# Performance work log

Hardware: AMD Instinct MI355X
Metric: run time of the kernel (lower is better)

## Reference

```python
import jax, jax.numpy as jnp
import numpy as np

B, L, DIM = 2, 1024, 512
HEADS = 8
D = DIM // HEADS
FORE_DIM, POST_DIM = 256, 1024
L_FORE, L_POST = 4 * L, L // 4


def setup_inputs() -> dict:
    key = jax.random.key(0)
    ks = jax.random.split(key, 8)
    s = 0.02  # weight init scale
    return {
        "x": jax.random.normal(ks[0], (B, L, DIM), jnp.float32),
        "fore_x": jax.random.normal(ks[1], (B, L_FORE, FORE_DIM), jnp.float32),
        "post_x": jax.random.normal(ks[2], (B, L_POST, POST_DIM), jnp.float32),
        # Linear weights stored [in, out] (transposed vs torch nn.Linear)
        "wq": jax.random.normal(ks[3], (DIM, DIM), jnp.float32) * s,
        "bq": jnp.zeros((DIM,), jnp.float32),
        "wkv1": jax.random.normal(ks[4], (FORE_DIM, 2 * DIM), jnp.float32) * s,
        "bkv1": jnp.zeros((2 * DIM,), jnp.float32),
        "wkv2": jax.random.normal(ks[5], (POST_DIM, 2 * DIM), jnp.float32) * s,
        "bkv2": jnp.zeros((2 * DIM,), jnp.float32),
        "wproj": jax.random.normal(ks[6], (3 * DIM, DIM), jnp.float32) * s,
        "bproj": jnp.zeros((DIM,), jnp.float32),
    }


def reference(x, fore_x, post_x, wq, bq, wkv1, bkv1, wkv2, bkv2, wproj, bproj):
    scale = D ** (-0.5)
    # q: [B, H, L, D], pre-scaled as in the torch code
    q = (x @ wq + bq).reshape(B, L, HEADS, D).transpose(0, 2, 1, 3) * scale

    def cross_attn(ctx, w, b):
        # ctx: [B, Lc, Cin] -> k, v: [B, H, Lc, D]
        kv = (ctx @ w + b).reshape(B, ctx.shape[1], 2, HEADS, D)
        k = kv[:, :, 0].transpose(0, 2, 1, 3)
        v = kv[:, :, 1].transpose(0, 2, 1, 3)
        attn = jax.nn.softmax(jnp.einsum("bhqd,bhkd->bhqk", q, k), axis=-1)
        out = jnp.einsum("bhqk,bhkd->bhqd", attn, v)
        return out.transpose(0, 2, 1, 3).reshape(B, L, DIM)

    x_2 = cross_attn(post_x, wkv2, bkv2)
    x_1 = cross_attn(fore_x, wkv1, bkv1)
    cat = jnp.concatenate([x, x_1, x_2], axis=2)  # [B, L, 3*DIM]
    return cat @ wproj + bproj
```

## Files before the change

kernel.cpp:

```cpp
#include <hip/hip_runtime.h>
#include <hip/hip_bf16.h>
#include <stdint.h>

typedef __attribute__((ext_vector_type(8))) short bf8;
typedef __attribute__((ext_vector_type(4))) short bf4;
typedef __attribute__((ext_vector_type(2))) short bf2;
typedef __attribute__((ext_vector_type(4))) float f32x4;

__device__ inline short f2bf(float f) {
  union { __hip_bfloat16 h; short s; } u;
  u.h = __float2bfloat16(f);
  return u.s;
}
__device__ inline float bf2f(short s) {
  union { short s; __hip_bfloat16 h; } u;
  u.s = s;
  return __bfloat162float(u.h);
}

__device__ inline f32x4 mfma16(bf8 a, bf8 b, f32x4 c) {
  return __builtin_amdgcn_mfma_f32_16x16x32_bf16(a, b, c, 0, 0, 0);
}

__global__ __launch_bounds__(256) void mega1_k(
    const float* __restrict__ x, const float* __restrict__ fore,
    const float* __restrict__ post,
    const float* __restrict__ wq, const float* __restrict__ bq,
    const float* __restrict__ wkv1, const float* __restrict__ bkv1,
    const float* __restrict__ wkv2, const float* __restrict__ bkv2,
    const float* __restrict__ wproj,
    short* __restrict__ qb, short* __restrict__ kv1, short* __restrict__ kv2,
    short* __restrict__ cat, short* __restrict__ wT)
{
  __shared__ __align__(16) short a_lds[2][128 * 40];
  __shared__ __align__(16) short b_lds[2][64 * 40];
  const int bid = blockIdx.x, tid = threadIdx.x;

  if (bid >= 1216) {
    float (*tl)[65] = reinterpret_cast<float(*)[65]>(&a_lds[0][0]);
    int tb = bid - 1216;
    int kt = tb % 24, nt = tb / 24;
    int k0 = kt * 64, n0 = nt * 64;
    int kr = tid >> 2, c4 = tid & 3;
#pragma unroll
    for (int i = 0; i < 4; ++i) {
      int cc = c4 + i * 4;
      float4 v = *(const float4*)&wproj[(size_t)(k0 + kr) * 512 + n0 + cc * 4];
      tl[kr][cc * 4 + 0] = v.x; tl[kr][cc * 4 + 1] = v.y;
      tl[kr][cc * 4 + 2] = v.z; tl[kr][cc * 4 + 3] = v.w;
    }
    __syncthreads();
    int nr = tid >> 2, p = tid & 3;
#pragma unroll
    for (int i = 0; i < 2; ++i) {
      int kk = p * 16 + i * 8;
      bf8 o;
#pragma unroll
      for (int j = 0; j < 8; ++j) o[j] = f2bf(tl[kk + j][nr]);
      *(bf8*)&wT[(size_t)(n0 + nr) * 1536 + k0 + kk] = o;
    }
    return;
  }

  const float *A, *W, *bias;
  short* out;
  int N, lda, ldo, m0, n0, K;
  float osc = 1.f;
  bool wcat = false;
  if (bid < 64) {
    A = post; W = wkv2; bias = bkv2; out = kv2;
    N = 1024; lda = 1024; ldo = 1024; K = 1024;
    m0 = (bid >> 4) * 128; n0 = (bid & 15) * 64;
  } else if (bid < 192) {
    int j = bid - 64;
    A = x; W = wq; bias = bq; out = qb;
    N = 512; lda = 512; ldo = 512; K = 512;
    m0 = (j >> 3) * 128; n0 = (j & 7) * 64;
    osc = 0.125f * 1.44269504088896f;
    wcat = (j & 7) == 0;
  } else {
    int j = bid - 192;
    A = fore; W = wkv1; bias = bkv1; out = kv1;
    N = 1024; lda = 256; ldo = 1024; K = 256;
    m0 = (j >> 4) * 128; n0 = (j & 15) * 64;
  }

  const int w = tid >> 6, lane = tid & 63, g = lane >> 4, lr = lane & 15;
  const int wrow = w & 1, wcol = w >> 1;

  f32x4 z = {0.f, 0.f, 0.f, 0.f};
  f32x4 acc[4][2];
#pragma unroll
  for (int mi = 0; mi < 4; ++mi)
#pragma unroll
    for (int ni = 0; ni < 2; ++ni) acc[mi][ni] = z;

  const int arow = tid >> 3, ac4 = tid & 7;
  const int bcol = tid & 63, bj4 = tid >> 6;

  float4 ra[4], rna[4];
  float rw[8], rnw[8];

  auto LOADA = [&](int kg, float4* af, float* wg) {
#pragma unroll
    for (int i = 0; i < 4; ++i)
      af[i] = *(const float4*)&A[(size_t)(m0 + arow + 32 * i) * lda + kg + ac4 * 4];
#pragma unroll
    for (int j = 0; j < 8; ++j)
      wg[j] = W[(size_t)(kg + bj4 * 8 + j) * N + n0 + bcol];
  };
  auto STAGE = [&](int b, const float4* af, const float* wg, int kg) {
#pragma unroll
    for (int i = 0; i < 4; ++i) {
      int rr = arow + 32 * i;
      int s = (ac4 >> 1) ^ (rr & 3);
      bf4 o;
      o[0] = f2bf(af[i].x); o[1] = f2bf(af[i].y);
      o[2] = f2bf(af[i].z); o[3] = f2bf(af[i].w);
      *(bf4*)&a_lds[b][rr * 40 + s * 8 + (ac4 & 1) * 4] = o;
      if (wcat)
        *(bf4*)&cat[(size_t)(m0 + rr) * 1536 + kg + ac4 * 4] = o;
    }
    int s = bj4 ^ (bcol & 3);
    bf8 o;
#pragma unroll
    for (int j = 0; j < 8; ++j) o[j] = f2bf(wg[j]);
    *(bf8*)&b_lds[b][bcol * 40 + s * 8] = o;
  };

  const int nit = K >> 5;
  LOADA(0, ra, rw);
  STAGE(0, ra, rw, 0);
  LOADA(32, rna, rnw);
  __syncthreads();

  for (int it = 0; it < nit; ++it) {
    if (it + 1 < nit) STAGE((it + 1) & 1, rna, rnw, (it + 1) * 32);
    if (it + 2 < nit) LOADA((it + 2) * 32, rna, rnw);

    const int b = it & 1;
    bf8 afr[4], bfr[2];
#pragma unroll
    for (int mi = 0; mi < 4; ++mi) {
      int row = wrow * 64 + mi * 16 + lr;
      afr[mi] = *(const bf8*)&a_lds[b][row * 40 + ((g ^ (row & 3)) << 3)];
    }
#pragma unroll
    for (int ni = 0; ni < 2; ++ni) {
      int col = wcol * 32 + ni * 16 + lr;
      bfr[ni] = *(const bf8*)&b_lds[b][col * 40 + ((g ^ (col & 3)) << 3)];
    }
#pragma unroll
    for (int mi = 0; mi < 4; ++mi)
#pragma unroll
      for (int ni = 0; ni < 2; ++ni)
        acc[mi][ni] = mfma16(afr[mi], bfr[ni], acc[mi][ni]);
    __syncthreads();
  }

#pragma unroll
  for (int ni = 0; ni < 2; ++ni) {
    int col = n0 + wcol * 32 + ni * 16 + lr;
    float bv = bias[col];
#pragma unroll
    for (int mi = 0; mi < 4; ++mi) {
      int rowb = m0 + wrow * 64 + mi * 16 + g * 4;
#pragma unroll
      for (int r = 0; r < 4; ++r)
        out[(size_t)(rowb + r) * ldo + col] = f2bf((acc[mi][ni][r] + bv) * osc);
    }
  }
}

__global__ __launch_bounds__(256) void attn_k(
    const short* __restrict__ q,
    const short* __restrict__ kv1, const short* __restrict__ kv2,
    short* __restrict__ o1, float* __restrict__ l1,
    short* __restrict__ cat)
{
  __shared__ __align__(16) short k_lds[64 * 64];
  __shared__ __align__(16) short v_lds[64 * 72];
  const int tid = threadIdx.x;
  const int w = tid >> 6, lane = tid & 63, g = lane >> 4, lr = lane & 15;

  const int bid = blockIdx.x;
  const short* kvsrc;
  int qt, h, bb, split, chunk, Lc;
  bool direct;
  if (bid < 1024) {
    qt = bid >> 7; int j = bid & 127;
    h = j & 7; int zz = j >> 3;
    bb = zz >> 3; split = zz & 7;
    kvsrc = kv1; chunk = 512; Lc = 4096; direct = false;
  } else {
    int j2 = bid - 1024;
    qt = j2 >> 4; int r = j2 & 15;
    h = r & 7; bb = r >> 3; split = 0;
    kvsrc = kv2; chunk = 256; Lc = 256; direct = true;
  }

  const int qbase = bb * 1024 + qt * 128 + w * 32;
  bf8 qfA[2], qfB[2];
#pragma unroll
  for (int s2 = 0; s2 < 2; ++s2) {
    const short* qp = &q[(size_t)(qbase + s2 * 16 + lr) * 512 + h * 64];
    qfA[s2] = *(const bf8*)&qp[g * 8];
    qfB[s2] = *(const bf8*)&qp[32 + g * 8];
  }

  const f32x4 z = {0.f, 0.f, 0.f, 0.f};
  f32x4 oaccT[2][4];
#pragma unroll
  for (int s2 = 0; s2 < 2; ++s2)
#pragma unroll
    for (int i = 0; i < 4; ++i) oaccT[s2][i] = z;
  float lsum_l[2] = {0.f, 0.f};

  const short* kvb = kvsrc + (size_t)bb * Lc * 1024 + (size_t)split * chunk * 1024;

  const int krow = tid >> 2, ksl = tid & 3;
  const short* kgp = kvb + (size_t)krow * 1024 + h * 64;
  const int vi = tid & 31, vj = tid >> 5;
  const short* vgp = kvb + (size_t)(2 * vi) * 1024 + 512 + h * 64 + vj * 8;
  const int lc0 = 2 * vi;
  const int vpos = (lc0 & 32) + ((lc0 & 12) << 1) + ((lc0 & 16) >> 2) + (lc0 & 3);

  bf8 k0c, k1c, v0c, v1c;
  k0c = *(const bf8*)(kgp + ksl * 8);
  k1c = *(const bf8*)(kgp + (ksl + 4) * 8);
  v0c = *(const bf8*)vgp;
  v1c = *(const bf8*)(vgp + 1024);

  const int nit = chunk >> 6;
  for (int it = 0; it < nit; ++it) {
    __syncthreads();
    *(bf8*)&k_lds[krow * 64 + ((ksl ^ (krow & 7)) << 3)] = k0c;
    *(bf8*)&k_lds[krow * 64 + (((ksl + 4) ^ (krow & 7)) << 3)] = k1c;
#pragma unroll
    for (int jj = 0; jj < 8; ++jj) {
      int d = vj * 8 + jj;
      bf2 pr; pr[0] = v0c[jj]; pr[1] = v1c[jj];
      *(bf2*)&v_lds[d * 72 + vpos] = pr;
    }
    __syncthreads();
    if (it + 1 < nit) {
      size_t off = (size_t)64 * 1024 * (it + 1);
      k0c = *(const bf8*)(kgp + off + ksl * 8);
      k1c = *(const bf8*)(kgp + off + (ksl + 4) * 8);
      v0c = *(const bf8*)(vgp + off);
      v1c = *(const bf8*)(vgp + off + 1024);
    }

    f32x4 sv[2][4];
#pragma unroll
    for (int t = 0; t < 4; ++t) {
      int lc = t * 16 + lr;
      bf8 kf0 = *(const bf8*)&k_lds[lc * 64 + ((g ^ (lc & 7)) << 3)];
      bf8 kf1 = *(const bf8*)&k_lds[lc * 64 + (((4 + g) ^ (lc & 7)) << 3)];
#pragma unroll
      for (int s2 = 0; s2 < 2; ++s2) {
        sv[s2][t] = mfma16(kf0, qfA[s2], z);
        sv[s2][t] = mfma16(kf1, qfB[s2], sv[s2][t]);
      }
    }

    bf8 pb[2][2];
#pragma unroll
    for (int s2 = 0; s2 < 2; ++s2) {
      float acc_l = 0.f;
#pragma unroll
      for (int t = 0; t < 4; ++t) {
        float p0 = exp2f(sv[s2][t][0]);
        float p1 = exp2f(sv[s2][t][1]);
        float p2 = exp2f(sv[s2][t][2]);
        float p3 = exp2f(sv[s2][t][3]);
        acc_l += (p0 + p1) + (p2 + p3);
        int c = t >> 1, hb = (t & 1) * 4;
        pb[s2][c][hb + 0] = f2bf(p0);
        pb[s2][c][hb + 1] = f2bf(p1);
        pb[s2][c][hb + 2] = f2bf(p2);
        pb[s2][c][hb + 3] = f2bf(p3);
      }
      lsum_l[s2] += acc_l;
    }

#pragma unroll
    for (int dt = 0; dt < 4; ++dt) {
      int d = dt * 16 + lr;
      bf8 vf0 = *(const bf8*)&v_lds[d * 72 + 8 * g];
      bf8 vf1 = *(const bf8*)&v_lds[d * 72 + 32 + 8 * g];
      oaccT[0][dt] = mfma16(vf0, pb[0][0], oaccT[0][dt]);
      oaccT[0][dt] = mfma16(vf1, pb[0][1], oaccT[0][dt]);
      oaccT[1][dt] = mfma16(vf0, pb[1][0], oaccT[1][dt]);
      oaccT[1][dt] = mfma16(vf1, pb[1][1], oaccT[1][dt]);
    }
  }

  if (direct) {
#pragma unroll
    for (int s2 = 0; s2 < 2; ++s2) {
      float t = lsum_l[s2];
      t += __shfl_xor(t, 16);
      t += __shfl_xor(t, 32);
      float rle = 1.f / t;
      int qrow = qbase + s2 * 16 + lr;
#pragma unroll
      for (int dt = 0; dt < 4; ++dt) {
        bf4 o4;
#pragma unroll
        for (int r = 0; r < 4; ++r) o4[r] = f2bf(oaccT[s2][dt][r] * rle);
        *(bf4*)&cat[(size_t)qrow * 1536 + 1024 + h * 64 + dt * 16 + 4 * g] = o4;
      }
    }
    return;
  }

#pragma unroll
  for (int s2 = 0; s2 < 2; ++s2) {
    int prow = (bb * 8 + h) * 1024 + qt * 128 + w * 32 + s2 * 16 + lr;
    short* ob = o1 + ((size_t)split * 16384 + prow) * 64;
#pragma unroll
    for (int dt = 0; dt < 4; ++dt) {
      bf4 o4;
#pragma unroll
      for (int r = 0; r < 4; ++r) o4[r] = f2bf(oaccT[s2][dt][r]);
      *(bf4*)&ob[dt * 16 + 4 * g] = o4;
    }
    float t = lsum_l[s2];
    t += __shfl_xor(t, 16);
    t += __shfl_xor(t, 32);
    if (g == 0) l1[(size_t)split * 16384 + prow] = t;
  }
}

__global__ __launch_bounds__(256) void comb_k(
    const short* __restrict__ o1, const float* __restrict__ l1,
    short* __restrict__ cat)
{
  int row = blockIdx.x * 32 + (threadIdx.x >> 3);
  int d8 = (threadIdx.x & 7) * 8;
  float l = 0.f;
#pragma unroll
  for (int s = 0; s < 8; ++s) l += l1[(size_t)s * 16384 + row];
  float acc[8] = {};
#pragma unroll
  for (int s = 0; s < 8; ++s) {
    bf8 v = *(const bf8*)&o1[((size_t)s * 16384 + row) * 64 + d8];
#pragma unroll
    for (int j = 0; j < 8; ++j) acc[j] += bf2f(v[j]);
  }
  float rle = 1.f / l;
  bf8 o;
#pragma unroll
  for (int j = 0; j < 8; ++j) o[j] = f2bf(acc[j] * rle);
  int bb = row >> 13, h = (row >> 10) & 7, qr = row & 1023;
  *(bf8*)&cat[(size_t)(bb * 1024 + qr) * 1536 + 512 + h * 64 + d8] = o;
}

__global__ __launch_bounds__(256) void gemmo_k(
    const short* __restrict__ A, const short* __restrict__ wT,
    const float* __restrict__ bias, float* __restrict__ out)
{
  __shared__ __align__(16) short a_lds[2][64 * 40];
  __shared__ __align__(16) short b_lds[2][64 * 40];
  const int tid = threadIdx.x;
  const int w = tid >> 6, lane = tid & 63, g = lane >> 4, lr = lane & 15;
  const int id = blockIdx.x;
  const int m = ((id >> 3) & 3) | ((id & 7) << 2);
  const int n = id >> 5;
  const int m0 = m * 64, n0 = n * 64;
  const int K = 1536;

  f32x4 z = {0.f, 0.f, 0.f, 0.f};
  f32x4 acc[4];
#pragma unroll
  for (int mi = 0; mi < 4; ++mi) acc[mi] = z;

  const int arow = tid >> 2, ac8 = tid & 3;
  const int bcol = tid & 63, bj4 = tid >> 6;
  bf8 ra, rna, rb, rnb;

  auto LOADAB = [&](int kg, bf8& ab, bf8& bb) {
    ab = *(const bf8*)&A[(size_t)(m0 + arow) * K + kg + ac8 * 8];
    bb = *(const bf8*)&wT[(size_t)(n0 + bcol) * K + kg + bj4 * 8];
  };
  auto STAGE = [&](int b, bf8 ab, bf8 bb) {
    *(bf8*)&a_lds[b][arow * 40 + ((ac8 ^ (arow & 3)) << 3)] = ab;
    *(bf8*)&b_lds[b][bcol * 40 + ((bj4 ^ (bcol & 3)) << 3)] = bb;
  };

  const int nit = K >> 5;
  LOADAB(0, ra, rb);
  STAGE(0, ra, rb);
  LOADAB(32, rna, rnb);
  __syncthreads();

  for (int it = 0; it < nit; ++it) {
    if (it + 1 < nit) STAGE((it + 1) & 1, rna, rnb);
    if (it + 2 < nit) LOADAB((it + 2) * 32, rna, rnb);

    const int b = it & 1;
    bf8 afr[4], bfr;
#pragma unroll
    for (int mi = 0; mi < 4; ++mi) {
      int row = mi * 16 + lr;
      afr[mi] = *(const bf8*)&a_lds[b][row * 40 + ((g ^ (row & 3)) << 3)];
    }
    {
      int col = w * 16 + lr;
      bfr = *(const bf8*)&b_lds[b][col * 40 + ((g ^ (col & 3)) << 3)];
    }
#pragma unroll
    for (int mi = 0; mi < 4; ++mi) acc[mi] = mfma16(afr[mi], bfr, acc[mi]);
    __syncthreads();
  }

  {
    int col = n0 + w * 16 + lr;
    float bv = bias[col];
#pragma unroll
    for (int mi = 0; mi < 4; ++mi) {
      int rowb = m0 + mi * 16 + g * 4;
#pragma unroll
      for (int r = 0; r < 4; ++r)
        out[(size_t)(rowb + r) * 512 + col] = acc[mi][r] + bv;
    }
  }
}

extern "C" void kernel_launch(void* const* d_in, const int* in_sizes, int n_in,
                              void* d_out, int out_size, void* d_ws, size_t ws_size,
                              hipStream_t stream) {
  const float* x     = (const float*)d_in[0];
  const float* fore  = (const float*)d_in[1];
  const float* post  = (const float*)d_in[2];
  const float* wq    = (const float*)d_in[3];
  const float* bq    = (const float*)d_in[4];
  const float* wkv1  = (const float*)d_in[5];
  const float* bkv1  = (const float*)d_in[6];
  const float* wkv2  = (const float*)d_in[7];
  const float* bkv2  = (const float*)d_in[8];
  const float* wproj = (const float*)d_in[9];
  const float* bproj = (const float*)d_in[10];

  char* ws = (char*)d_ws;
  short* qb  = (short*)ws;
  short* kv1 = (short*)(ws + (2ull << 20));
  short* kv2 = (short*)(ws + (18ull << 20));
  short* cat = (short*)(ws + (19ull << 20));
  short* o1  = (short*)(ws + (25ull << 20));
  float* l1  = (float*)(ws + (41ull << 20));
  short* wT  = (short*)(ws + (42ull << 20));

  mega1_k<<<1408, 256, 0, stream>>>(x, fore, post, wq, bq, wkv1, bkv1,
                                    wkv2, bkv2, wproj, qb, kv1, kv2, cat, wT);
  attn_k<<<1152, 256, 0, stream>>>(qb, kv1, kv2, o1, l1, cat);
  comb_k<<<512, 256, 0, stream>>>(o1, l1, cat);
  gemmo_k<<<256, 256, 0, stream>>>(cat, wT, bproj, (float*)d_out);
}
```

Measured before the change: 86.05 us.

## Pre-convert activations and weights to bf16 in a separate kernel before projection GEMMs

Adds a conversion kernel that turns x, fore_x and post_x into bf16 buffers, writes the x slice of cat, and transposes all weight matrices into bf16 [N,K] layout. The projection GEMM then loads 16-byte bf16 vectors for both operands, replacing strided scalar fp32 weight loads and in-loop conversion. The cost is an extra kernel launch plus extra global write and reread traffic for the converted copies (roughly 7 MB of bf16 data).

```diff
diff --git a/kernel.cpp b/kernel.cpp
--- a/kernel.cpp
+++ b/kernel.cpp
@@ -22,66 +22,103 @@
   return __builtin_amdgcn_mfma_f32_16x16x32_bf16(a, b, c, 0, 0, 0);
 }
 
-__global__ __launch_bounds__(256) void mega1_k(
+__global__ __launch_bounds__(256) void cvtw_k(
     const float* __restrict__ x, const float* __restrict__ fore,
     const float* __restrict__ post,
-    const float* __restrict__ wq, const float* __restrict__ bq,
-    const float* __restrict__ wkv1, const float* __restrict__ bkv1,
-    const float* __restrict__ wkv2, const float* __restrict__ bkv2,
-    const float* __restrict__ wproj,
-    short* __restrict__ qb, short* __restrict__ kv1, short* __restrict__ kv2,
-    short* __restrict__ cat, short* __restrict__ wT)
+    const float* __restrict__ wq, const float* __restrict__ wkv1,
+    const float* __restrict__ wkv2, const float* __restrict__ wproj,
+    short* __restrict__ xb, short* __restrict__ fb, short* __restrict__ pb,
+    short* __restrict__ cat,
+    short* __restrict__ wqT, short* __restrict__ wkv1T,
+    short* __restrict__ wkv2T, short* __restrict__ wT)
+{
+  __shared__ float tl[64][65];
+  const int bid = blockIdx.x, tid = threadIdx.x;
+  if (bid < 576) {
+    const float* Win; short* WT; int K, N, kt, nt;
+    if (bid < 64)       { Win = wq;    WT = wqT;   K = 512;  N = 512;  kt = bid >> 3;  nt = bid & 7; }
+    else if (bid < 128) { int j = bid - 64;  Win = wkv1;  WT = wkv1T; K = 256;  N = 1024; kt = j >> 4; nt = j & 15; }
+    else if (bid < 384) { int j = bid - 128; Win = wkv2;  WT = wkv2T; K = 1024; N = 1024; kt = j >> 4; nt = j & 15; }
+    else                { int j = bid - 384; Win = wproj; WT = wT;    K = 1536; N = 512;  kt = j % 24; nt = j / 24; }
+    const int k0 = kt * 64, n0 = nt * 64;
+    const int kr = tid >> 2, c4 = tid & 3;
+#pragma unroll
+    for (int i = 0; i < 4; ++i) {
+      int cc = c4 + i * 4;
+      float4 v = *(const float4*)&Win[(size_t)(k0 + kr) * N + n0 + cc * 4];
+      tl[kr][cc * 4 + 0] = v.x; tl[kr][cc * 4 + 1] = v.y;
+      tl[kr][cc * 4 + 2] = v.z; tl[kr][cc * 4 + 3] = v.w;
+    }
+    __syncthreads();
+    const int nr = tid >> 2, p = tid & 3;
+#pragma unroll
+    for (int i = 0; i < 2; ++i) {
+      int kk = p * 16 + i * 8;
+      bf8 o;
+#pragma unroll
+      for (int j = 0; j < 8; ++j) o[j] = f2bf(tl[kk + j][nr]);
+      *(bf8*)&WT[(size_t)(n0 + nr) * K + k0 + kk] = o;
+    }
+    return;
+  }
+  int e0 = (bid - 576) * 1024 + tid;
+#pragma unroll
+  for (int i = 0; i < 4; ++i) {
+    int q4 = e0 + 256 * i;
+    float4 v;
+    bf4 o;
+    if (q4 < 262144) {
+      v = ((const float4*)x)[q4];
+      o[0] = f2bf(v.x); o[1] = f2bf(v.y); o[2] = f2bf(v.z); o[3] = f2bf(v.w);
+      ((bf4*)xb)[q4] = o;
+      int row = q4 >> 7, col = (q4 & 127) * 4;
+      *(bf4*)&cat[(size_t)row * 1536 + col] = o;
+    } else if (q4 < 786432) {
+      int j = q4 - 262144;
+      v = ((const float4*)fore)[j];
+      o[0] = f2bf(v.x); o[1] = f2bf(v.y); o[2] = f2bf(v.z); o[3] = f2bf(v.w);
+      ((bf4*)fb)[j] = o;
+    } else {
+      int j = q4 - 786432;
+      v = ((const float4*)post)[j];
+      o[0] = f2bf(v.x); o[1] = f2bf(v.y); o[2] = f2bf(v.z); o[3] = f2bf(v.w);
+      ((bf4*)pb)[j] = o;
+    }
+  }
+}
+
+__global__ __launch_bounds__(256) void mega1_k(
+    const short* __restrict__ xb, const short* __restrict__ fb,
+    const short* __restrict__ pb,
+    const short* __restrict__ wqT, const short* __restrict__ wkv1T,
+    const short* __restrict__ wkv2T,
+    const float* __restrict__ bq, const float* __restrict__ bkv1,
+    const float* __restrict__ bkv2,
+    short* __restrict__ qb, short* __restrict__ kv1, short* __restrict__ kv2)
 {
   __shared__ __align__(16) short a_lds[2][128 * 40];
   __shared__ __align__(16) short b_lds[2][64 * 40];
   const int bid = blockIdx.x, tid = threadIdx.x;
 
-  if (bid >= 1216) {
-    float (*tl)[65] = reinterpret_cast<float(*)[65]>(&a_lds[0][0]);
-    int tb = bid - 1216;
-    int kt = tb % 24, nt = tb / 24;
-    int k0 = kt * 64, n0 = nt * 64;
-    int kr = tid >> 2, c4 = tid & 3;
-#pragma unroll
-    for (int i = 0; i < 4; ++i) {
-      int cc = c4 + i * 4;
-      float4 v = *(const float4*)&wproj[(size_t)(k0 + kr) * 512 + n0 + cc * 4];
-      tl[kr][cc * 4 + 0] = v.x; tl[kr][cc * 4 + 1] = v.y;
-      tl[kr][cc * 4 + 2] = v.z; tl[kr][cc * 4 + 3] = v.w;
-    }
-    __syncthreads();
-    int nr = tid >> 2, p = tid & 3;
-#pragma unroll
-    for (int i = 0; i < 2; ++i) {
-      int kk = p * 16 + i * 8;
-      bf8 o;
-#pragma unroll
-      for (int j = 0; j < 8; ++j) o[j] = f2bf(tl[kk + j][nr]);
-      *(bf8*)&wT[(size_t)(n0 + nr) * 1536 + k0 + kk] = o;
-    }
-    return;
-  }
-
-  const float *A, *W, *bias;
+  const short *A, *WT;
+  const float* bias;
   short* out;
-  int N, lda, ldo, m0, n0, K;
+  int K, N, m0, n0;
   float osc = 1.f;
-  bool wcat = false;
   if (bid < 64) {
-    A = post; W = wkv2; bias = bkv2; out = kv2;
-    N = 1024; lda = 1024; ldo = 1024; K = 1024;
+    A = pb; WT = wkv2T; bias = bkv2; out = kv2;
+    K = 1024; N = 1024;
     m0 = (bid >> 4) * 128; n0 = (bid & 15) * 64;
   } else if (bid < 192) {
     int j = bid - 64;
-    A = x; W = wq; bias = bq; out = qb;
-    N = 512; lda = 512; ldo = 512; K = 512;
+    A = xb; WT = wqT; bias = bq; out = qb;
+    K = 512; N = 512;
     m0 = (j >> 3) * 128; n0 = (j & 7) * 64;
     osc = 0.125f * 1.44269504088896f;
-    wcat = (j & 7) == 0;
   } else {
     int j = bid - 192;
-    A = fore; W = wkv1; bias = bkv1; out = kv1;
-    N = 1024; lda = 256; ldo = 1024; K = 256;
+    A = fb; WT = wkv1T; bias = bkv1; out = kv1;
+    K = 256; N = 1024;
     m0 = (j >> 4) * 128; n0 = (j & 15) * 64;
   }
 
@@ -95,48 +132,32 @@
 #pragma unroll
     for (int ni = 0; ni < 2; ++ni) acc[mi][ni] = z;
 
-  const int arow = tid >> 3, ac4 = tid & 7;
-  const int bcol = tid & 63, bj4 = tid >> 6;
-
-  float4 ra[4], rna[4];
-  float rw[8], rnw[8];
-
-  auto LOADA = [&](int kg, float4* af, float* wg) {
-#pragma unroll
-    for (int i = 0; i < 4; ++i)
-      af[i] = *(const float4*)&A[(size_t)(m0 + arow + 32 * i) * lda + kg + ac4 * 4];
-#pragma unroll
-    for (int j = 0; j < 8; ++j)
-      wg[j] = W[(size_t)(kg + bj4 * 8 + j) * N + n0 + bcol];
+  const int arow = tid >> 2, ac8 = tid & 3;
+  const int bcol = tid >> 2, bks = tid & 3;
+
+  bf8 ra[2], rna[2], rb, rnb;
+
+  auto LOADAB = [&](int kg, bf8* a, bf8& b) {
+    a[0] = *(const bf8*)&A[(size_t)(m0 + arow) * K + kg + ac8 * 8];
+    a[1] = *(const bf8*)&A[(size_t)(m0 + arow + 64) * K + kg + ac8 * 8];
+    b = *(const bf8*)&WT[(size_t)(n0 + bcol) * K + kg + bks * 8];
   };
-  auto STAGE = [&](int b, const float4* af, const float* wg, int kg) {
-#pragma unroll
-    for (int i = 0; i < 4; ++i) {
-      int rr = arow + 32 * i;
-      int s = (ac4 >> 1) ^ (rr & 3);
-      bf4 o;
-      o[0] = f2bf(af[i].x); o[1] = f2bf(af[i].y);
-      o[2] = f2bf(af[i].z); o[3] = f2bf(af[i].w);
-      *(bf4*)&a_lds[b][rr * 40 + s * 8 + (ac4 & 1) * 4] = o;
-      if (wcat)
-        *(bf4*)&cat[(size_t)(m0 + rr) * 1536 + kg + ac4 * 4] = o;
-    }
-    int s = bj4 ^ (bcol & 3);
-    bf8 o;
-#pragma unroll
-    for (int j = 0; j < 8; ++j) o[j] = f2bf(wg[j]);
-    *(bf8*)&b_lds[b][bcol * 40 + s * 8] = o;
+  auto STAGE = [&](int b_, const bf8* a, bf8 b) {
+    *(bf8*)&a_lds[b_][arow * 40 + ((ac8 ^ (arow & 3)) << 3)] = a[0];
+    int r2 = arow + 64;
+    *(bf8*)&a_lds[b_][r2 * 40 + ((ac8 ^ (r2 & 3)) << 3)] = a[1];
+    *(bf8*)&b_lds[b_][bcol * 40 + ((bks ^ (bcol & 3)) << 3)] = b;
   };
 
   const int nit = K >> 5;
-  LOADA(0, ra, rw);
-  STAGE(0, ra, rw, 0);
-  LOADA(32, rna, rnw);
+  LOADAB(0, ra, rb);
+  STAGE(0, ra, rb);
+  LOADAB(32, rna, rnb);
   __syncthreads();
 
   for (int it = 0; it < nit; ++it) {
-    if (it + 1 < nit) STAGE((it + 1) & 1, rna, rnw, (it + 1) * 32);
-    if (it + 2 < nit) LOADA((it + 2) * 32, rna, rnw);
+    if (it + 1 < nit) STAGE((it + 1) & 1, rna, rnb);
+    if (it + 2 < nit) LOADAB((it + 2) * 32, rna, rnb);
 
     const int b = it & 1;
     bf8 afr[4], bfr[2];
@@ -167,7 +188,7 @@
       int rowb = m0 + wrow * 64 + mi * 16 + g * 4;
 #pragma unroll
       for (int r = 0; r < 4; ++r)
-        out[(size_t)(rowb + r) * ldo + col] = f2bf((acc[mi][ni][r] + bv) * osc);
+        out[(size_t)(rowb + r) * N + col] = f2bf((acc[mi][ni][r] + bv) * osc);
     }
   }
 }
@@ -264,7 +285,7 @@
       }
     }
 
-    bf8 pb[2][2];
+    bf8 pb2[2][2];
 #pragma unroll
     for (int s2 = 0; s2 < 2; ++s2) {
       float acc_l = 0.f;
@@ -276,10 +297,10 @@
         float p3 = exp2f(sv[s2][t][3]);
         acc_l += (p0 + p1) + (p2 + p3);
         int c = t >> 1, hb = (t & 1) * 4;
-        pb[s2][c][hb + 0] = f2bf(p0);
-        pb[s2][c][hb + 1] = f2bf(p1);
-        pb[s2][c][hb + 2] = f2bf(p2);
-        pb[s2][c][hb + 3] = f2bf(p3);
+        pb2[s2][c][hb + 0] = f2bf(p0);
+        pb2[s2][c][hb + 1] = f2bf(p1);
+        pb2[s2][c][hb + 2] = f2bf(p2);
+        pb2[s2][c][hb + 3] = f2bf(p3);
       }
       lsum_l[s2] += acc_l;
     }
@@ -289,10 +310,10 @@
       int d = dt * 16 + lr;
       bf8 vf0 = *(const bf8*)&v_lds[d * 72 + 8 * g];
       bf8 vf1 = *(const bf8*)&v_lds[d * 72 + 32 + 8 * g];
-      oaccT[0][dt] = mfma16(vf0, pb[0][0], oaccT[0][dt]);
-      oaccT[0][dt] = mfma16(vf1, pb[0][1], oaccT[0][dt]);
-      oaccT[1][dt] = mfma16(vf0, pb[1][0], oaccT[1][dt]);
-      oaccT[1][dt] = mfma16(vf1, pb[1][1], oaccT[1][dt]);
+      oaccT[0][dt] = mfma16(vf0, pb2[0][0], oaccT[0][dt]);
+      oaccT[0][dt] = mfma16(vf1, pb2[0][1], oaccT[0][dt]);
+      oaccT[1][dt] = mfma16(vf0, pb2[1][0], oaccT[1][dt]);
+      oaccT[1][dt] = mfma16(vf1, pb2[1][1], oaccT[1][dt]);
     }
   }
 
@@ -444,16 +465,24 @@
   const float* bproj = (const float*)d_in[10];
 
   char* ws = (char*)d_ws;
-  short* qb  = (short*)ws;
-  short* kv1 = (short*)(ws + (2ull << 20));
-  short* kv2 = (short*)(ws + (18ull << 20));
-  short* cat = (short*)(ws + (19ull << 20));
-  short* o1  = (short*)(ws + (25ull << 20));
-  float* l1  = (float*)(ws + (41ull << 20));
-  short* wT  = (short*)(ws + (42ull << 20));
-
-  mega1_k<<<1408, 256, 0, stream>>>(x, fore, post, wq, bq, wkv1, bkv1,
-                                    wkv2, bkv2, wproj, qb, kv1, kv2, cat, wT);
+  short* qb     = (short*)ws;
+  short* kv1    = (short*)(ws + (2ull << 20));
+  short* kv2    = (short*)(ws + (18ull << 20));
+  short* cat    = (short*)(ws + (19ull << 20));
+  short* o1     = (short*)(ws + (25ull << 20));
+  float* l1     = (float*)(ws + (41ull << 20));
+  short* wT     = (short*)(ws + (42ull << 20));
+  short* xb     = (short*)(ws + (44ull << 20));
+  short* fb     = (short*)(ws + (46ull << 20));
+  short* pb     = (short*)(ws + (50ull << 20));
+  short* wqT    = (short*)(ws + (51ull << 20));
+  short* wkv1T  = (short*)(ws + (52ull << 20));
+  short* wkv2T  = (short*)(ws + (53ull << 20));
+
+  cvtw_k<<<1472, 256, 0, stream>>>(x, fore, post, wq, wkv1, wkv2, wproj,
+                                   xb, fb, pb, cat, wqT, wkv1T, wkv2T, wT);
+  mega1_k<<<1216, 256, 0, stream>>>(xb, fb, pb, wqT, wkv1T, wkv2T,
+                                    bq, bkv1, bkv2, qb, kv1, kv2);
   attn_k<<<1152, 256, 0, stream>>>(qb, kv1, kv2, o1, l1, cat);
   comb_k<<<512, 256, 0, stream>>>(o1, l1, cat);
   gemmo_k<<<256, 256, 0, stream>>>(cat, wT, bproj, (float*)d_out);
```

Measured after the change: 85.90 us (median of 2 runs). About the same (-0.2%).
